# Kernel tuning notes

Hardware: AMD Instinct MI355X
Metric: run time of the kernel (lower is better)

The kernel has to match this reference:

```python
import jax, jax.numpy as jnp
import numpy as np

GRID_LO = 32
GRID_HI = 128
NF = 4          # n_features
K = 9           # num_neighbors
NUM_CLASSES = 36
BS = 128
P_LO = GRID_LO * GRID_LO   # 1024
P_HI = GRID_HI * GRID_HI   # 16384


def _knn_neighbor_indices():
    """Replicates cKDTree(lo_coords).query(hi_coords, k=K)[1]: lo grid has
    spacing ratio=grid_hi//grid_lo, hi grid spacing 1; neighbors sorted by
    distance (stable sort -> ties broken by lower linear index)."""
    ratio = GRID_HI // GRID_LO
    lo = np.stack(np.meshgrid(np.arange(GRID_LO) * ratio,
                              np.arange(GRID_LO) * ratio, indexing='ij'),
                  axis=-1).reshape(-1, 2).astype(np.float64)   # (P_LO, 2)
    hi = np.stack(np.meshgrid(np.arange(GRID_HI),
                              np.arange(GRID_HI), indexing='ij'),
                  axis=-1).reshape(-1, 2).astype(np.float64)   # (P_HI, 2)
    d2 = ((hi[:, None, :] - lo[None, :, :]) ** 2).sum(-1)      # (P_HI, P_LO)
    idx = np.argsort(d2, axis=1, kind='stable')[:, :K]          # (P_HI, K)
    return jnp.asarray(idx, dtype=jnp.int32)


def setup_inputs() -> dict:
    key = jax.random.key(0)
    k1, k2, k3, k4, k5 = jax.random.split(key, 5)
    x = jax.random.normal(k1, (BS, NF * P_LO), dtype=jnp.float32)
    cls_ids = jax.random.randint(k2, (BS,), 0, NUM_CLASSES)
    neighbor_indices = _knn_neighbor_indices()                  # (P_HI, K)
    weight_map = jax.random.normal(k3, (NUM_CLASSES, NF, P_HI, K), dtype=jnp.float32) * 0.05
    bias_low = jax.random.normal(k4, (NUM_CLASSES, NF, P_LO), dtype=jnp.float32) * 0.05
    bias_high = jax.random.normal(k5, (NUM_CLASSES, NF, P_HI), dtype=jnp.float32) * 0.05
    return {"x": x, "cls_ids": cls_ids, "neighbor_indices": neighbor_indices,
            "weight_map": weight_map, "bias_low": bias_low, "bias_high": bias_high}


def reference(x, cls_ids, neighbor_indices, weight_map, bias_low, bias_high):
    # x: (BS, NF*P_LO) -> (BS, NF, P_LO)
    y_low = x.reshape(x.shape[0], NF, P_LO)
    y_low_db = y_low - bias_low[cls_ids]                        # (BS, NF, P_LO)
    # gather k=9 lo-res neighbors for every hi-res pixel (all features at once)
    neigh = y_low_db[:, :, neighbor_indices]                    # (BS, NF, P_HI, K)
    weights = weight_map[cls_ids]                               # (BS, NF, P_HI, K)
    out = jnp.einsum('bfpk,bfpk->bfp', neigh, weights)          # weighted sum over k
    out = out + bias_high[cls_ids]                              # (BS, NF, P_HI)
    return out.reshape(x.shape[0], NF, GRID_HI, GRID_HI)
```

## Files before the change

kernel.cpp:

```cpp
#include <hip/hip_runtime.h>

#define BS      128
#define NF      4
#define NC      36
#define P_LO    1024
#define P_HI    16384
#define KNN     9
#define THREADS 256
#define TILE_P  256
#define NTILES  (P_HI / TILE_P)
#define LIST_OFF 64
#define SCHED_OFF 36
#define SLICE   192

__global__ __launch_bounds__(128) void build_lists_kernel(
    const int* __restrict__ cls_ids, int* __restrict__ ws)
{
    __shared__ int cnt[NC];
    __shared__ int pk[9];
    const int t = threadIdx.x;
    if (t < NC) cnt[t] = 0;
    if (t >= 64 && t < 73) pk[t - 64] = 0;
    __syncthreads();
    if (t < BS) {
        int c = cls_ids[t];
        int pos = atomicAdd(&cnt[c], 1);
        ws[LIST_OFF + c * BS + pos] = t;
    }
    __syncthreads();
    if (t < NC) {
        int ct = cnt[t];
        ws[t] = ct;
        int r = 0;
        for (int j = 0; j < NC; ++j) {
            int cj = cnt[j];
            r += (cj > ct) || (cj == ct && j < t);
        }
        atomicOr(&pk[r >> 2], t << ((r & 3) << 3));
    }
    __syncthreads();
    if (t < 9) ws[SCHED_OFF + t] = pk[t];
}

__global__ __launch_bounds__(THREADS) void rect_up_kernel(
    const float* __restrict__ x,
    const int*   __restrict__ ws,
    const int*   __restrict__ nbr,
    const float* __restrict__ wmap,
    const float* __restrict__ blo,
    const float* __restrict__ bhi,
    float*       __restrict__ out)
{
    __shared__ __align__(16) float ybuf[2][SLICE][4];

    const int tile = blockIdx.x & (NTILES - 1);
    const int rank = blockIdx.x >> 6;
    const int cls  = (ws[SCHED_OFF + (rank >> 2)] >> ((rank & 3) << 3)) & 0xFF;
    const int n_b  = ws[cls];
    if (n_b == 0) return;

    const int tid = threadIdx.x;
    const int p   = tile * TILE_P + tid;
    const int m   = tile >> 1;
    const int base32 = (min(max(m - 2, 0), 26)) << 5;
    const int s   = tid >> 6;
    const int qq  = tid & 63;

    const int* list = ws + LIST_OFF + cls * BS;
    const int R  = (n_b + 3) >> 2;
    const int NP = NF * R;

#define WAVE_ID(rr) ((4 * (rr) + s < n_b) ? list[4 * (rr) + s] : list[4 * (rr)])
#define LOAD_XP(dst, ff, rr) {                                               \
        const int id_ = WAVE_ID(rr);                                         \
        const float* xp_ = x + ((size_t)id_ * NF + (ff)) * P_LO + base32 + qq; \
        dst[0] = xp_[0]; dst[1] = xp_[64]; dst[2] = xp_[128]; }

    int nbl[KNN];
    {
        const int* ir = nbr + (size_t)p * KNN;
        #pragma unroll
        for (int k = 0; k < KNN; ++k) nbl[k] = ir[k] - base32;
    }
    float w_[KNN];
    {
        const float* wr = wmap + ((size_t)cls * NF * P_HI + p) * KNN;
        #pragma unroll
        for (int k = 0; k < KNN; ++k) w_[k] = wr[k];
    }
    float bhc;
    {
        float t = bhi[(size_t)cls * NF * P_HI + p];
        const float* blp = blo + (size_t)cls * NF * P_LO + base32;
        #pragma unroll
        for (int k = 0; k < KNN; ++k) t = fmaf(-w_[k], blp[nbl[k]], t);
        bhc = t;
    }

    float xp1[3], xp2[3], xp3[3];
    {
        float x0[3];
        LOAD_XP(x0, 0, 0);
        LOAD_XP(xp1, 1 / R, 1 % R);
        LOAD_XP(xp2, 2 / R, 2 % R);
        LOAD_XP(xp3, 3 / R, 3 % R);
        #pragma unroll
        for (int t = 0; t < 3; ++t) ybuf[0][qq + 64 * t][s] = x0[t];
    }
    asm volatile("s_waitcnt lgkmcnt(0)" ::: "memory");
    __builtin_amdgcn_s_barrier();

    int pb = 0, f = 0, r = 0;
    int f3 = 4 / R, r3 = 4 % R;
    float wn[KNN], bhn = 0.f;

    for (int ph = 0; ph < NP; ++ph) {
        const int s0  = 4 * r;
        const int id0 = list[s0];
        const int id1 = (s0 + 1 < n_b) ? list[s0 + 1] : id0;
        const int id2 = (s0 + 2 < n_b) ? list[s0 + 2] : id0;
        const int id3 = (s0 + 3 < n_b) ? list[s0 + 3] : id0;

        if (ph + 1 < NP) {
            #pragma unroll
            for (int t = 0; t < 3; ++t) ybuf[pb ^ 1][qq + 64 * t][s] = xp1[t];
        }

        #pragma unroll
        for (int t = 0; t < 3; ++t) { xp1[t] = xp2[t]; xp2[t] = xp3[t]; }
        if (f3 < NF) LOAD_XP(xp3, f3, r3);

        float blgn[KNN];
        const bool fb = (r == 0) && (f + 1 < NF);
        if (fb) {
            const float* wrn = wmap + ((size_t)(cls * NF + f + 1) * P_HI + p) * KNN;
            #pragma unroll
            for (int k = 0; k < KNN; ++k) wn[k] = wrn[k];
            const float* blpn = blo + (size_t)(cls * NF + f + 1) * P_LO + base32;
            #pragma unroll
            for (int k = 0; k < KNN; ++k) blgn[k] = blpn[nbl[k]];
            bhn = bhi[(size_t)(cls * NF + f + 1) * P_HI + p];
        }

        const float* yb = &ybuf[pb][0][0];
        float a0 = 0.f, a1 = 0.f, a2 = 0.f, a3 = 0.f;
        #pragma unroll
        for (int k = 0; k < KNN; ++k) {
            const float4 yv = *(const float4*)(yb + 4 * nbl[k]);
            a0 = fmaf(w_[k], yv.x, a0);
            a1 = fmaf(w_[k], yv.y, a1);
            a2 = fmaf(w_[k], yv.z, a2);
            a3 = fmaf(w_[k], yv.w, a3);
        }

        out[((size_t)id0 * NF + f) * P_HI + p] = a0 + bhc;
        out[((size_t)id1 * NF + f) * P_HI + p] = a1 + bhc;
        out[((size_t)id2 * NF + f) * P_HI + p] = a2 + bhc;
        out[((size_t)id3 * NF + f) * P_HI + p] = a3 + bhc;

        if (fb) {
            float t = bhn;
            #pragma unroll
            for (int k = 0; k < KNN; ++k) t = fmaf(-wn[k], blgn[k], t);
            bhn = t;
        }

        if (ph + 1 < NP) {
            asm volatile("s_waitcnt lgkmcnt(0)" ::: "memory");
            __builtin_amdgcn_s_barrier();
        }
        pb ^= 1;
        if (++r == R) {
            r = 0; ++f;
            #pragma unroll
            for (int k = 0; k < KNN; ++k) w_[k] = wn[k];
            bhc = bhn;
        }
        if (++r3 == R) { r3 = 0; ++f3; }
    }
#undef LOAD_XP
#undef WAVE_ID
}

extern "C" void kernel_launch(void* const* d_in, const int* in_sizes, int n_in,
                              void* d_out, int out_size, void* d_ws, size_t ws_size,
                              hipStream_t stream) {
    const float* x    = (const float*)d_in[0];
    const int*   cls  = (const int*)d_in[1];
    const int*   nbr  = (const int*)d_in[2];
    const float* wmap = (const float*)d_in[3];
    const float* blo  = (const float*)d_in[4];
    const float* bhi  = (const float*)d_in[5];
    float*       out  = (float*)d_out;
    int*         wsl  = (int*)d_ws;

    build_lists_kernel<<<1, 128, 0, stream>>>(cls, wsl);
    rect_up_kernel<<<NC * NTILES, THREADS, 0, stream>>>(
        x, wsl, nbr, wmap, blo, bhi, out);
}
```

Before: 163.5 us.

## Split work per wave by feature and 64-pixel tile, drop block barriers

Each wavefront now handles one (class, feature, 64-pixel tile) unit on its own, with a private LDS slice, instead of a 256-thread block cycling over features and batch groups with block-wide barriers. The x slices for the next batch group are prefetched into registers, and only a wave-local LDS wait separates iterations. This gives four times as many parallel work units and removes s_barrier synchronisation. In exchange, neighbor indices, the nbr and bias-correction loads and the x slice are now fetched per feature and per wave rather than shared across a block, and the cross-feature weight prefetch is gone.

```diff
diff --git a/kernel.cpp b/kernel.cpp
--- a/kernel.cpp
+++ b/kernel.cpp
@@ -7,8 +7,8 @@
 #define P_HI    16384
 #define KNN     9
 #define THREADS 256
-#define TILE_P  256
-#define NTILES  (P_HI / TILE_P)
+#define WTILE   64
+#define NTILES  (P_HI / WTILE)
 #define LIST_OFF 64
 #define SCHED_OFF 36
 #define SLICE   192
@@ -51,30 +51,26 @@
     const float* __restrict__ bhi,
     float*       __restrict__ out)
 {
-    __shared__ __align__(16) float ybuf[2][SLICE][4];
+    __shared__ __align__(16) float ybuf[4][SLICE][4];
 
-    const int tile = blockIdx.x & (NTILES - 1);
-    const int rank = blockIdx.x >> 6;
+    const int tid  = threadIdx.x;
+    const int wv   = tid >> 6;
+    const int lane = tid & 63;
+    const int u    = (blockIdx.x << 2) | wv;
+    const int tile = u & (NTILES - 1);
+    const int fr   = u >> 8;
+    const int f    = fr & (NF - 1);
+    const int rank = fr >> 2;
     const int cls  = (ws[SCHED_OFF + (rank >> 2)] >> ((rank & 3) << 3)) & 0xFF;
     const int n_b  = ws[cls];
     if (n_b == 0) return;
 
-    const int tid = threadIdx.x;
-    const int p   = tile * TILE_P + tid;
-    const int m   = tile >> 1;
-    const int base32 = (min(max(m - 2, 0), 26)) << 5;
-    const int s   = tid >> 6;
-    const int qq  = tid & 63;
+    const int p      = tile * WTILE + lane;
+    const int m      = p >> 9;
+    const int base32 = min(max(m - 2, 0), 26) << 5;
 
     const int* list = ws + LIST_OFF + cls * BS;
-    const int R  = (n_b + 3) >> 2;
-    const int NP = NF * R;
-
-#define WAVE_ID(rr) ((4 * (rr) + s < n_b) ? list[4 * (rr) + s] : list[4 * (rr)])
-#define LOAD_XP(dst, ff, rr) {                                               \
-        const int id_ = WAVE_ID(rr);                                         \
-        const float* xp_ = x + ((size_t)id_ * NF + (ff)) * P_LO + base32 + qq; \
-        dst[0] = xp_[0]; dst[1] = xp_[64]; dst[2] = xp_[128]; }
+    const int R = (n_b + 3) >> 2;
 
     int nbl[KNN];
     {
@@ -84,102 +80,90 @@
     }
     float w_[KNN];
     {
-        const float* wr = wmap + ((size_t)cls * NF * P_HI + p) * KNN;
+        const float* wr = wmap + ((size_t)(cls * NF + f) * P_HI + p) * KNN;
         #pragma unroll
         for (int k = 0; k < KNN; ++k) w_[k] = wr[k];
     }
-    float bhc;
+    float bhc = bhi[(size_t)(cls * NF + f) * P_HI + p];
     {
-        float t = bhi[(size_t)cls * NF * P_HI + p];
-        const float* blp = blo + (size_t)cls * NF * P_LO + base32;
+        const float* blp = blo + (size_t)(cls * NF + f) * P_LO + base32;
         #pragma unroll
-        for (int k = 0; k < KNN; ++k) t = fmaf(-w_[k], blp[nbl[k]], t);
-        bhc = t;
+        for (int k = 0; k < KNN; ++k) bhc = fmaf(-w_[k], blp[nbl[k]], bhc);
     }
 
-    float xp1[3], xp2[3], xp3[3];
+    int id0 = list[0];
+    int id1 = (1 < n_b) ? list[1] : id0;
+    int id2 = (2 < n_b) ? list[2] : id0;
+    int id3 = (3 < n_b) ? list[3] : id0;
+
+    float xv[12];
     {
-        float x0[3];
-        LOAD_XP(x0, 0, 0);
-        LOAD_XP(xp1, 1 / R, 1 % R);
-        LOAD_XP(xp2, 2 / R, 2 % R);
-        LOAD_XP(xp3, 3 / R, 3 % R);
+        const float* b0 = x + ((size_t)id0 * NF + f) * P_LO + base32 + lane;
+        const float* b1 = x + ((size_t)id1 * NF + f) * P_LO + base32 + lane;
+        const float* b2 = x + ((size_t)id2 * NF + f) * P_LO + base32 + lane;
+        const float* b3 = x + ((size_t)id3 * NF + f) * P_LO + base32 + lane;
         #pragma unroll
-        for (int t = 0; t < 3; ++t) ybuf[0][qq + 64 * t][s] = x0[t];
+        for (int t = 0; t < 3; ++t) {
+            xv[t]     = b0[t << 6];
+            xv[3 + t] = b1[t << 6];
+            xv[6 + t] = b2[t << 6];
+            xv[9 + t] = b3[t << 6];
+        }
     }
-    asm volatile("s_waitcnt lgkmcnt(0)" ::: "memory");
-    __builtin_amdgcn_s_barrier();
 
-    int pb = 0, f = 0, r = 0;
-    int f3 = 4 / R, r3 = 4 % R;
-    float wn[KNN], bhn = 0.f;
+    for (int r = 0; r < R; ++r) {
+        if (r) asm volatile("s_waitcnt lgkmcnt(0)" ::: "memory");
 
-    for (int ph = 0; ph < NP; ++ph) {
-        const int s0  = 4 * r;
-        const int id0 = list[s0];
-        const int id1 = (s0 + 1 < n_b) ? list[s0 + 1] : id0;
-        const int id2 = (s0 + 2 < n_b) ? list[s0 + 2] : id0;
-        const int id3 = (s0 + 3 < n_b) ? list[s0 + 3] : id0;
-
-        if (ph + 1 < NP) {
-            #pragma unroll
-            for (int t = 0; t < 3; ++t) ybuf[pb ^ 1][qq + 64 * t][s] = xp1[t];
+        #pragma unroll
+        for (int t = 0; t < 3; ++t) {
+            float4 v;
+            v.x = xv[t]; v.y = xv[3 + t]; v.z = xv[6 + t]; v.w = xv[9 + t];
+            *(float4*)&ybuf[wv][lane + (t << 6)][0] = v;
         }
 
-        #pragma unroll
-        for (int t = 0; t < 3; ++t) { xp1[t] = xp2[t]; xp2[t] = xp3[t]; }
-        if (f3 < NF) LOAD_XP(xp3, f3, r3);
+        const int c0 = id0, c1 = id1, c2 = id2, c3 = id3;
 
-        float blgn[KNN];
-        const bool fb = (r == 0) && (f + 1 < NF);
-        if (fb) {
-            const float* wrn = wmap + ((size_t)(cls * NF + f + 1) * P_HI + p) * KNN;
+        float xn[12];
+        if (r + 1 < R) {
+            const int s = 4 * (r + 1);
+            id0 = list[s];
+            id1 = (s + 1 < n_b) ? list[s + 1] : id0;
+            id2 = (s + 2 < n_b) ? list[s + 2] : id0;
+            id3 = (s + 3 < n_b) ? list[s + 3] : id0;
+            const float* b0 = x + ((size_t)id0 * NF + f) * P_LO + base32 + lane;
+            const float* b1 = x + ((size_t)id1 * NF + f) * P_LO + base32 + lane;
+            const float* b2 = x + ((size_t)id2 * NF + f) * P_LO + base32 + lane;
+            const float* b3 = x + ((size_t)id3 * NF + f) * P_LO + base32 + lane;
             #pragma unroll
-            for (int k = 0; k < KNN; ++k) wn[k] = wrn[k];
-            const float* blpn = blo + (size_t)(cls * NF + f + 1) * P_LO + base32;
-            #pragma unroll
-            for (int k = 0; k < KNN; ++k) blgn[k] = blpn[nbl[k]];
-            bhn = bhi[(size_t)(cls * NF + f + 1) * P_HI + p];
+            for (int t = 0; t < 3; ++t) {
+                xn[t]     = b0[t << 6];
+                xn[3 + t] = b1[t << 6];
+                xn[6 + t] = b2[t << 6];
+                xn[9 + t] = b3[t << 6];
+            }
         }
 
-        const float* yb = &ybuf[pb][0][0];
+        const float* yb = &ybuf[wv][0][0];
         float a0 = 0.f, a1 = 0.f, a2 = 0.f, a3 = 0.f;
         #pragma unroll
         for (int k = 0; k < KNN; ++k) {
-            const float4 yv = *(const float4*)(yb + 4 * nbl[k]);
+            const float4 yv = *(const float4*)(yb + (nbl[k] << 2));
             a0 = fmaf(w_[k], yv.x, a0);
             a1 = fmaf(w_[k], yv.y, a1);
             a2 = fmaf(w_[k], yv.z, a2);
             a3 = fmaf(w_[k], yv.w, a3);
         }
 
-        out[((size_t)id0 * NF + f) * P_HI + p] = a0 + bhc;
-        out[((size_t)id1 * NF + f) * P_HI + p] = a1 + bhc;
-        out[((size_t)id2 * NF + f) * P_HI + p] = a2 + bhc;
-        out[((size_t)id3 * NF + f) * P_HI + p] = a3 + bhc;
+        out[((size_t)c0 * NF + f) * P_HI + p] = a0 + bhc;
+        out[((size_t)c1 * NF + f) * P_HI + p] = a1 + bhc;
+        out[((size_t)c2 * NF + f) * P_HI + p] = a2 + bhc;
+        out[((size_t)c3 * NF + f) * P_HI + p] = a3 + bhc;
 
-        if (fb) {
-            float t = bhn;
+        if (r + 1 < R) {
             #pragma unroll
-            for (int k = 0; k < KNN; ++k) t = fmaf(-wn[k], blgn[k], t);
-            bhn = t;
+            for (int t = 0; t < 12; ++t) xv[t] = xn[t];
         }
-
-        if (ph + 1 < NP) {
-            asm volatile("s_waitcnt lgkmcnt(0)" ::: "memory");
-            __builtin_amdgcn_s_barrier();
-        }
-        pb ^= 1;
-        if (++r == R) {
-            r = 0; ++f;
-            #pragma unroll
-            for (int k = 0; k < KNN; ++k) w_[k] = wn[k];
-            bhc = bhn;
-        }
-        if (++r3 == R) { r3 = 0; ++f3; }
     }
-#undef LOAD_XP
-#undef WAVE_ID
 }
 
 extern "C" void kernel_launch(void* const* d_in, const int* in_sizes, int n_in,
@@ -195,6 +179,6 @@
     int*         wsl  = (int*)d_ws;
 
     build_lists_kernel<<<1, 128, 0, stream>>>(cls, wsl);
-    rect_up_kernel<<<NC * NTILES, THREADS, 0, stream>>>(
+    rect_up_kernel<<<NC * NF * NTILES / 4, THREADS, 0, stream>>>(
         x, wsl, nbr, wmap, blo, bhi, out);
 }
```

Measured after the change: 163.2 us. No clear change (-0.2%).
